# Performance work log

Hardware: AMD Instinct MI355X
Metric: run time of the kernel (lower is better)

The kernel has to match this reference:

```python
import jax, jax.numpy as jnp
import numpy as np

WINDOW_SIZE = 128

def setup_inputs() -> dict:
    key = jax.random.key(0)
    kq, kk, kv = jax.random.split(key, 3)
    B, S, D = 4, 4096, 128
    q = jax.random.normal(kq, (B, S, D), dtype=jnp.float32)
    k = jax.random.normal(kk, (B, S, D), dtype=jnp.float32)
    v = jax.random.normal(kv, (B, S, D), dtype=jnp.float32)
    return {"q": q, "k": k, "v": v}

def reference(q, k, v):
    B, S, D = q.shape
    q = q / jnp.sqrt(jnp.asarray(D, q.dtype))
    # band mask: tril(window_size-1) & triu(-(window_size-1)) == |i - j| <= window_size-1
    i = jax.lax.broadcasted_iota(jnp.int32, (S, S), 0)
    j = jax.lax.broadcasted_iota(jnp.int32, (S, S), 1)
    mask = jnp.abs(i - j) <= (WINDOW_SIZE - 1)
    scores = jnp.einsum('bqd,bkd->bqk', q, k)  # [B,S,S]
    scores = jnp.where(mask, scores, jnp.asarray(-1e9, scores.dtype))
    weights = jax.nn.softmax(scores, axis=-1)
    return jnp.einsum('bqk,bkd->bqd', weights, v)
```

## Files before the change

### kernel.cpp

```cpp
#include <hip/hip_runtime.h>


typedef __attribute__((ext_vector_type(8))) _Float16 half8;
typedef __attribute__((ext_vector_type(2))) __fp16 fp16x2;
typedef __attribute__((ext_vector_type(4))) float floatx4;

#define MFMA_F16(a, b, c) __builtin_amdgcn_mfma_f32_16x16x32_f16(a, b, c, 0, 0, 0)

constexpr int S_ = 4096, D_ = 128, W_ = 127;
constexpr int BQ = 64, BK = 64;
constexpr int PST = 72;
constexpr int OST = 132;

union SMem {
  struct {
    _Float16 Kh[2][BK * D_];
    _Float16 Vt[2][D_ * BK];
    _Float16 Ps[4][16 * PST];
  } a;
  struct {
    float Om[8][16 * OST];
    float l_[8][16];
  } b;
};

__device__ __forceinline__ unsigned pk2(float a, float b) {
  union { fp16x2 h; unsigned u; } c;
  c.h = __builtin_amdgcn_cvt_pkrtz(a, b);
  return c.u;
}

__device__ __forceinline__ void gll16(const _Float16* g, _Float16* l) {
  __builtin_amdgcn_global_load_lds(
      (const __attribute__((address_space(1))) void*)g,
      (__attribute__((address_space(3))) void*)l, 16, 0, 0);
}

__global__ __launch_bounds__(256, 4)
void prep_kernel(const float* __restrict__ kg, const float* __restrict__ vg,
                 _Float16* __restrict__ K16, _Float16* __restrict__ Vt16)
{
  __shared__ __align__(16) _Float16 Vs[BK * D_];
  const int t  = threadIdx.x;
  const int bb = blockIdx.x >> 6;
  const int c  = blockIdx.x & 63;
  const size_t base = ((size_t)bb * S_ + c * 64) * D_;

#pragma unroll
  for (int j = 0; j < 4; ++j) {
    const int id = t + 256 * j;
    const int s = id >> 4, blk = id & 15;
    const float* src = kg + base + s * D_ + blk * 8;
    float4 a  = *(const float4*)src;
    float4 b2 = *(const float4*)(src + 4);
    uint4 w;
    w.x = pk2(a.x, a.y);  w.y = pk2(a.z, a.w);
    w.z = pk2(b2.x, b2.y); w.w = pk2(b2.z, b2.w);
    *(uint4*)(K16 + base + s * D_ + 8 * (blk ^ (s & 7))) = w;
  }

  const int vr = t >> 5, vc = t & 31;
  float4 vf[8];
#pragma unroll
  for (int u = 0; u < 8; ++u)
    vf[u] = *(const float4*)(vg + base + (8 * vr + u) * D_ + 4 * vc);
#pragma unroll
  for (int i = 0; i < 4; ++i) {
    uint4 tv;
    tv.x = pk2(((const float*)&vf[0])[i], ((const float*)&vf[1])[i]);
    tv.y = pk2(((const float*)&vf[2])[i], ((const float*)&vf[3])[i]);
    tv.z = pk2(((const float*)&vf[4])[i], ((const float*)&vf[5])[i]);
    tv.w = pk2(((const float*)&vf[6])[i], ((const float*)&vf[7])[i]);
    const int d = 4 * vc + i;
    *(uint4*)(&Vs[d * 64 + 8 * (vr ^ (d & 7))]) = tv;
  }
  __syncthreads();
  _Float16* vdst = Vt16 + (size_t)(bb * 64 + c) * (D_ * 64);
#pragma unroll
  for (int i = 0; i < 4; ++i) {
    const int id2 = t + 256 * i;
    *(uint4*)(vdst + id2 * 8) = *(const uint4*)(&Vs[id2 * 8]);
  }
}

__global__ __launch_bounds__(512, 2)
void swa_v6_kernel(const float* __restrict__ qg,
                   const _Float16* __restrict__ K16,
                   const _Float16* __restrict__ Vt16,
                   float* __restrict__ og)
{
  __shared__ __align__(16) SMem sm;
  const int tid  = threadIdx.x;
  const int lane = tid & 63;
  const int wave = tid >> 6;
  const int lx   = lane & 15;
  const int quad = lane >> 4;
  const int tile = wave & 3;
  const int par  = wave >> 2;

  const int bid = blockIdx.x;
  const int lid = (bid & 7) * 32 + (bid >> 3);
  const int bb  = lid >> 6;
  const int q0  = (lid & 63) * BQ;

  const float* qb = qg + (size_t)bb * S_ * D_;
  float*       ob = og + (size_t)bb * S_ * D_;

  const int qrow = q0 + 16 * tile + lx;
  half8 qh[4], ql[4];
#pragma unroll
  for (int ks = 0; ks < 4; ++ks) {
    const float* p = qb + (size_t)qrow * D_ + 32 * ks + 8 * quad;
#pragma unroll
    for (int j = 0; j < 8; ++j) {
      float f = p[j];
      _Float16 h = (_Float16)f;
      qh[ks][j] = h;
      ql[ks][j] = (_Float16)(f - (float)h);
    }
  }

  floatx4 o[8];
#pragma unroll
  for (int dt = 0; dt < 8; ++dt) o[dt] = (floatx4){0.f, 0.f, 0.f, 0.f};
  float lp[4] = {0.f, 0.f, 0.f, 0.f};

  const int kstart = (q0 > W_) ? (q0 - W_) : 0;
  int kend = q0 + BQ - 1 + W_;
  if (kend > S_ - 1) kend = S_ - 1;
  const int c0 = kstart >> 6, c1 = kend >> 6;

  const int ilo = q0 + 16 * tile, ihi = ilo + 15;
  const float C1 = 0.12751727f, C2 = -5.7707802f;

  const int wk = (wave < 4) ? wave : (wave - 4);

  {
    const int b0 = c0 & 1;
    const _Float16* kcb = K16 + ((size_t)bb * S_ + c0 * 64) * D_;
    const _Float16* vcb = Vt16 + (size_t)(bb * 64 + c0) * (D_ * 64);
#pragma unroll
    for (int i = 0; i < 4; ++i) {
      const int ofs = (wk * 4 + i) * 512;
      if (wave < 4) gll16(kcb + ofs + lane * 8, &sm.a.Kh[b0][ofs]);
      else          gll16(vcb + ofs + lane * 8, &sm.a.Vt[b0][ofs]);
    }
  }

  for (int c = c0; c <= c1; ++c) {
    const int buf = c & 1;
    asm volatile("s_waitcnt vmcnt(0)" ::: "memory");
    __builtin_amdgcn_s_barrier();
    asm volatile("" ::: "memory");

    if (c < c1) {
      const _Float16* kcb = K16 + ((size_t)bb * S_ + (c + 1) * 64) * D_;
      const _Float16* vcb = Vt16 + (size_t)(bb * 64 + (c + 1)) * (D_ * 64);
#pragma unroll
      for (int i = 0; i < 4; ++i) {
        const int ofs = (wk * 4 + i) * 512;
        if (wave < 4) gll16(kcb + ofs + lane * 8, &sm.a.Kh[buf ^ 1][ofs]);
        else          gll16(vcb + ofs + lane * 8, &sm.a.Vt[buf ^ 1][ofs]);
      }
    }

    if (((c - c0) & 1) != par) continue;
    const int kc = c * BK;
    if (kc + BK - 1 < ilo - W_ || kc > ihi + W_) continue;

    floatx4 acc[4];
#pragma unroll
    for (int ct = 0; ct < 4; ++ct) acc[ct] = (floatx4){0.f, 0.f, 0.f, 0.f};
#pragma unroll
    for (int ks = 0; ks < 4; ++ks) {
#pragma unroll
      for (int ct = 0; ct < 4; ++ct) {
        const int row = 16 * ct + lx;
        half8 bfr = *(const half8*)(
            &sm.a.Kh[buf][row * D_ + 8 * ((4 * ks + quad) ^ (lx & 7))]);
        acc[ct] = MFMA_F16(qh[ks], bfr, acc[ct]);
        acc[ct] = MFMA_F16(ql[ks], bfr, acc[ct]);
      }
    }

    const int ibase = q0 + 16 * tile + 4 * quad;
#pragma unroll
    for (int r = 0; r < 4; ++r) {
      const int i = ibase + r;
      float psum = 0.f;
#pragma unroll
      for (int ct = 0; ct < 4; ++ct) {
        const int col = kc + 16 * ct + lx;
        const bool v = (unsigned)(col - i + W_) <= (unsigned)(2 * W_);
        const float e = __builtin_amdgcn_exp2f(__builtin_fmaf(acc[ct][r], C1, C2));
        const float p = v ? e : 0.f;
        psum += p;
        sm.a.Ps[tile][(4 * quad + r) * PST + 16 * ct + lx] = (_Float16)p;
      }
      lp[r] += psum;
    }
    asm volatile("s_waitcnt lgkmcnt(0)" ::: "memory");
    half8 pa0 = *(const half8*)(&sm.a.Ps[tile][lx * PST + 8 * quad]);
    half8 pa1 = *(const half8*)(&sm.a.Ps[tile][lx * PST + 32 + 8 * quad]);

#pragma unroll
    for (int dt = 0; dt < 8; ++dt) {
      const int d = 16 * dt + lx;
      half8 v0 = *(const half8*)(&sm.a.Vt[buf][d * 64 + 8 * (quad ^ (d & 7))]);
      half8 v1 = *(const half8*)(&sm.a.Vt[buf][d * 64 + 8 * ((4 + quad) ^ (d & 7))]);
      o[dt] = MFMA_F16(pa0, v0, o[dt]);
      o[dt] = MFMA_F16(pa1, v1, o[dt]);
    }
  }

#pragma unroll
  for (int r = 0; r < 4; ++r) {
    float s = lp[r];
    s += __shfl_xor(s, 1);
    s += __shfl_xor(s, 2);
    s += __shfl_xor(s, 4);
    s += __shfl_xor(s, 8);
    lp[r] = s;
  }

  __syncthreads();
#pragma unroll
  for (int dt = 0; dt < 8; ++dt)
#pragma unroll
    for (int r = 0; r < 4; ++r)
      sm.b.Om[wave][(4 * quad + r) * OST + 16 * dt + lx] = o[dt][r];
  if (lx == 0) {
#pragma unroll
    for (int r = 0; r < 4; ++r) sm.b.l_[wave][4 * quad + r] = lp[r];
  }
  __syncthreads();

  const int row = tid >> 3, cd = tid & 7;
  const int tl = row >> 4, r16 = row & 15;
  const float inv = 1.f / (sm.b.l_[tl][r16] + sm.b.l_[tl + 4][r16]);
  const float* Oa = &sm.b.Om[tl][r16 * OST + 16 * cd];
  const float* Ob = &sm.b.Om[tl + 4][r16 * OST + 16 * cd];
  float* dst = ob + (size_t)(q0 + row) * D_ + 16 * cd;
#pragma unroll
  for (int t = 0; t < 4; ++t) {
    float4 xa = *(const float4*)(Oa + 4 * t);
    float4 xb = *(const float4*)(Ob + 4 * t);
    float4 r4;
    r4.x = (xa.x + xb.x) * inv;
    r4.y = (xa.y + xb.y) * inv;
    r4.z = (xa.z + xb.z) * inv;
    r4.w = (xa.w + xb.w) * inv;
    *(float4*)(dst + 4 * t) = r4;
  }
}

extern "C" void kernel_launch(void* const* d_in, const int* in_sizes, int n_in,
                              void* d_out, int out_size, void* d_ws, size_t ws_size,
                              hipStream_t stream) {
  const float* q = (const float*)d_in[0];
  const float* k = (const float*)d_in[1];
  const float* v = (const float*)d_in[2];
  float* out = (float*)d_out;

  const int B = in_sizes[0] / (S_ * D_);
  _Float16* K16  = (_Float16*)d_ws;
  _Float16* Vt16 = (_Float16*)d_ws + (size_t)B * S_ * D_;

  prep_kernel<<<dim3(B * (S_ / BK)), dim3(256), 0, stream>>>(k, v, K16, Vt16);
  swa_v6_kernel<<<dim3(B * (S_ / BQ)), dim3(512), 0, stream>>>(q, K16, Vt16, out);
}
```

Baseline: 89.57 us.

## Fuse K/V fp16 conversion into attention kernel with register-staged prefetch

Removes the separate prep kernel that converted K and V to fp16 (with V transposed) in a global workspace. The attention kernel now loads fp32 K/V chunks into registers one chunk ahead, then converts, swizzles and writes them to LDS at the start of the next iteration. This drops one launch and a global round trip of the fp16 copies. In exchange each block redoes the conversion for its overlapping window (about three chunks per block), uses more registers, and puts more LDS-store work on the critical path. Q is now loaded with float4 vector loads.

```diff
diff --git a/kernel.cpp b/kernel.cpp
--- a/kernel.cpp
+++ b/kernel.cpp
@@ -30,63 +30,56 @@
   return c.u;
 }
 
-__device__ __forceinline__ void gll16(const _Float16* g, _Float16* l) {
-  __builtin_amdgcn_global_load_lds(
-      (const __attribute__((address_space(1))) void*)g,
-      (__attribute__((address_space(3))) void*)l, 16, 0, 0);
-}
-
-__global__ __launch_bounds__(256, 4)
-void prep_kernel(const float* __restrict__ kg, const float* __restrict__ vg,
-                 _Float16* __restrict__ K16, _Float16* __restrict__ Vt16)
-{
-  __shared__ __align__(16) _Float16 Vs[BK * D_];
-  const int t  = threadIdx.x;
-  const int bb = blockIdx.x >> 6;
-  const int c  = blockIdx.x & 63;
-  const size_t base = ((size_t)bb * S_ + c * 64) * D_;
-
-#pragma unroll
-  for (int j = 0; j < 4; ++j) {
-    const int id = t + 256 * j;
-    const int s = id >> 4, blk = id & 15;
-    const float* src = kg + base + s * D_ + blk * 8;
-    float4 a  = *(const float4*)src;
-    float4 b2 = *(const float4*)(src + 4);
-    uint4 w;
-    w.x = pk2(a.x, a.y);  w.y = pk2(a.z, a.w);
-    w.z = pk2(b2.x, b2.y); w.w = pk2(b2.z, b2.w);
-    *(uint4*)(K16 + base + s * D_ + 8 * (blk ^ (s & 7))) = w;
-  }
-
-  const int vr = t >> 5, vc = t & 31;
-  float4 vf[8];
-#pragma unroll
-  for (int u = 0; u < 8; ++u)
-    vf[u] = *(const float4*)(vg + base + (8 * vr + u) * D_ + 4 * vc);
-#pragma unroll
-  for (int i = 0; i < 4; ++i) {
-    uint4 tv;
-    tv.x = pk2(((const float*)&vf[0])[i], ((const float*)&vf[1])[i]);
-    tv.y = pk2(((const float*)&vf[2])[i], ((const float*)&vf[3])[i]);
-    tv.z = pk2(((const float*)&vf[4])[i], ((const float*)&vf[5])[i]);
-    tv.w = pk2(((const float*)&vf[6])[i], ((const float*)&vf[7])[i]);
-    const int d = 4 * vc + i;
-    *(uint4*)(&Vs[d * 64 + 8 * (vr ^ (d & 7))]) = tv;
-  }
-  __syncthreads();
-  _Float16* vdst = Vt16 + (size_t)(bb * 64 + c) * (D_ * 64);
-#pragma unroll
-  for (int i = 0; i < 4; ++i) {
-    const int id2 = t + 256 * i;
-    *(uint4*)(vdst + id2 * 8) = *(const uint4*)(&Vs[id2 * 8]);
-  }
-}
+#define ISSUE(cc) do {                                                        \
+    if (isK) {                                                                \
+      const float* kc_ = kb + (size_t)(cc) * (BK * D_);                       \
+      _Pragma("unroll")                                                       \
+      for (int j = 0; j < 4; ++j) {                                           \
+        const int id = tid + 256 * j;                                         \
+        const int s = id >> 4, blk = id & 15;                                 \
+        const float* src = kc_ + s * D_ + blk * 8;                            \
+        st[2 * j]     = *(const float4*)src;                                  \
+        st[2 * j + 1] = *(const float4*)(src + 4);                            \
+      }                                                                       \
+    } else {                                                                  \
+      const float* vc_ = vb + (size_t)(cc) * (BK * D_);                       \
+      _Pragma("unroll")                                                       \
+      for (int u = 0; u < 8; ++u)                                             \
+        st[u] = *(const float4*)(vc_ + (8 * vw + u) * D_ + 4 * vcg);          \
+    }                                                                         \
+  } while (0)
+
+#define COMMIT(bf) do {                                                       \
+    if (isK) {                                                                \
+      _Pragma("unroll")                                                       \
+      for (int j = 0; j < 4; ++j) {                                           \
+        const int id = tid + 256 * j;                                         \
+        const int s = id >> 4, blk = id & 15;                                 \
+        uint4 wv;                                                             \
+        wv.x = pk2(st[2 * j].x, st[2 * j].y);                                 \
+        wv.y = pk2(st[2 * j].z, st[2 * j].w);                                 \
+        wv.z = pk2(st[2 * j + 1].x, st[2 * j + 1].y);                         \
+        wv.w = pk2(st[2 * j + 1].z, st[2 * j + 1].w);                         \
+        *(uint4*)(&sm.a.Kh[bf][s * D_ + 8 * (blk ^ (s & 7))]) = wv;           \
+      }                                                                       \
+    } else {                                                                  \
+      _Pragma("unroll")                                                       \
+      for (int i = 0; i < 4; ++i) {                                           \
+        uint4 tv;                                                             \
+        tv.x = pk2(((const float*)&st[0])[i], ((const float*)&st[1])[i]);     \
+        tv.y = pk2(((const float*)&st[2])[i], ((const float*)&st[3])[i]);     \
+        tv.z = pk2(((const float*)&st[4])[i], ((const float*)&st[5])[i]);     \
+        tv.w = pk2(((const float*)&st[6])[i], ((const float*)&st[7])[i]);     \
+        const int d = 4 * vcg + i;                                            \
+        *(uint4*)(&sm.a.Vt[bf][d * 64 + 8 * (vw ^ (d & 7))]) = tv;            \
+      }                                                                       \
+    }                                                                         \
+  } while (0)
 
 __global__ __launch_bounds__(512, 2)
-void swa_v6_kernel(const float* __restrict__ qg,
-                   const _Float16* __restrict__ K16,
-                   const _Float16* __restrict__ Vt16,
+void swa_v7_kernel(const float* __restrict__ qg,
+                   const float* __restrict__ kg,
+                   const float* __restrict__ vg,
                    float* __restrict__ og)
 {
   __shared__ __align__(16) SMem sm;
@@ -104,19 +97,29 @@
   const int q0  = (lid & 63) * BQ;
 
   const float* qb = qg + (size_t)bb * S_ * D_;
+  const float* kb = kg + (size_t)bb * S_ * D_;
+  const float* vb = vg + (size_t)bb * S_ * D_;
   float*       ob = og + (size_t)bb * S_ * D_;
+
+  const bool isK = (wave < 4);
+  const int  t2  = tid & 255;
+  const int  vw  = t2 & 7;
+  const int  vcg = t2 >> 3;
+  float4 st[8];
 
   const int qrow = q0 + 16 * tile + lx;
   half8 qh[4], ql[4];
 #pragma unroll
   for (int ks = 0; ks < 4; ++ks) {
     const float* p = qb + (size_t)qrow * D_ + 32 * ks + 8 * quad;
+    float4 f0 = *(const float4*)p;
+    float4 f1 = *(const float4*)(p + 4);
+    float fa[8] = {f0.x, f0.y, f0.z, f0.w, f1.x, f1.y, f1.z, f1.w};
 #pragma unroll
     for (int j = 0; j < 8; ++j) {
-      float f = p[j];
-      _Float16 h = (_Float16)f;
+      _Float16 h = (_Float16)fa[j];
       qh[ks][j] = h;
-      ql[ks][j] = (_Float16)(f - (float)h);
+      ql[ks][j] = (_Float16)(fa[j] - (float)h);
     }
   }
 
@@ -133,36 +136,17 @@
   const int ilo = q0 + 16 * tile, ihi = ilo + 15;
   const float C1 = 0.12751727f, C2 = -5.7707802f;
 
-  const int wk = (wave < 4) ? wave : (wave - 4);
-
-  {
-    const int b0 = c0 & 1;
-    const _Float16* kcb = K16 + ((size_t)bb * S_ + c0 * 64) * D_;
-    const _Float16* vcb = Vt16 + (size_t)(bb * 64 + c0) * (D_ * 64);
-#pragma unroll
-    for (int i = 0; i < 4; ++i) {
-      const int ofs = (wk * 4 + i) * 512;
-      if (wave < 4) gll16(kcb + ofs + lane * 8, &sm.a.Kh[b0][ofs]);
-      else          gll16(vcb + ofs + lane * 8, &sm.a.Vt[b0][ofs]);
-    }
-  }
+  ISSUE(c0);
 
   for (int c = c0; c <= c1; ++c) {
     const int buf = c & 1;
-    asm volatile("s_waitcnt vmcnt(0)" ::: "memory");
+
+    COMMIT(buf);
+    asm volatile("s_waitcnt lgkmcnt(0)" ::: "memory");
     __builtin_amdgcn_s_barrier();
     asm volatile("" ::: "memory");
 
-    if (c < c1) {
-      const _Float16* kcb = K16 + ((size_t)bb * S_ + (c + 1) * 64) * D_;
-      const _Float16* vcb = Vt16 + (size_t)(bb * 64 + (c + 1)) * (D_ * 64);
-#pragma unroll
-      for (int i = 0; i < 4; ++i) {
-        const int ofs = (wk * 4 + i) * 512;
-        if (wave < 4) gll16(kcb + ofs + lane * 8, &sm.a.Kh[buf ^ 1][ofs]);
-        else          gll16(vcb + ofs + lane * 8, &sm.a.Vt[buf ^ 1][ofs]);
-      }
-    }
+    if (c < c1) ISSUE(c + 1);
 
     if (((c - c0) & 1) != par) continue;
     const int kc = c * BK;
@@ -257,15 +241,13 @@
 extern "C" void kernel_launch(void* const* d_in, const int* in_sizes, int n_in,
                               void* d_out, int out_size, void* d_ws, size_t ws_size,
                               hipStream_t stream) {
+  (void)d_ws; (void)ws_size;
   const float* q = (const float*)d_in[0];
   const float* k = (const float*)d_in[1];
   const float* v = (const float*)d_in[2];
   float* out = (float*)d_out;
 
   const int B = in_sizes[0] / (S_ * D_);
-  _Float16* K16  = (_Float16*)d_ws;
-  _Float16* Vt16 = (_Float16*)d_ws + (size_t)B * S_ * D_;
-
-  prep_kernel<<<dim3(B * (S_ / BK)), dim3(256), 0, stream>>>(k, v, K16, Vt16);
-  swa_v6_kernel<<<dim3(B * (S_ / BQ)), dim3(512), 0, stream>>>(q, K16, Vt16, out);
+
+  swa_v7_kernel<<<dim3(B * (S_ / BQ)), dim3(512), 0, stream>>>(q, k, v, out);
 }
```

New measurement: 92.00 us. 1.03x slower.

## Split each key chunk between wave groups by 32-key halves instead of alternating chunks

Applied to the files above, without the earlier changes.

Before, the two wave groups took alternating 64-key chunks, so when a block spans an odd number of chunks one group does more work than the other. Now both groups process every staged chunk, each computing QK^T, softmax weights and the PV product for its own 32-key half. The band-mask skip test also works at 32-key granularity, so halves that lie entirely outside a tile's window can be skipped. This trades halved MFMA work per chunk per wave for better balance between the groups and finer skipping, at the cost of less instruction-level work per barrier interval.

```diff
diff --git a/kernel.cpp b/kernel.cpp
--- a/kernel.cpp
+++ b/kernel.cpp
@@ -84,7 +84,7 @@
 }
 
 __global__ __launch_bounds__(512, 2)
-void swa_v6_kernel(const float* __restrict__ qg,
+void swa_v8_kernel(const float* __restrict__ qg,
                    const _Float16* __restrict__ K16,
                    const _Float16* __restrict__ Vt16,
                    float* __restrict__ og)
@@ -164,22 +164,23 @@
       }
     }
 
-    if (((c - c0) & 1) != par) continue;
     const int kc = c * BK;
-    if (kc + BK - 1 < ilo - W_ || kc > ihi + W_) continue;
-
-    floatx4 acc[4];
-#pragma unroll
-    for (int ct = 0; ct < 4; ++ct) acc[ct] = (floatx4){0.f, 0.f, 0.f, 0.f};
+    const int klo = kc + 32 * par;
+    if (klo + 31 < ilo - W_ || klo > ihi + W_) continue;
+
+    floatx4 acc[2];
+#pragma unroll
+    for (int h = 0; h < 2; ++h) acc[h] = (floatx4){0.f, 0.f, 0.f, 0.f};
 #pragma unroll
     for (int ks = 0; ks < 4; ++ks) {
 #pragma unroll
-      for (int ct = 0; ct < 4; ++ct) {
+      for (int h = 0; h < 2; ++h) {
+        const int ct = 2 * par + h;
         const int row = 16 * ct + lx;
         half8 bfr = *(const half8*)(
             &sm.a.Kh[buf][row * D_ + 8 * ((4 * ks + quad) ^ (lx & 7))]);
-        acc[ct] = MFMA_F16(qh[ks], bfr, acc[ct]);
-        acc[ct] = MFMA_F16(ql[ks], bfr, acc[ct]);
+        acc[h] = MFMA_F16(qh[ks], bfr, acc[h]);
+        acc[h] = MFMA_F16(ql[ks], bfr, acc[h]);
       }
     }
 
@@ -189,10 +190,11 @@
       const int i = ibase + r;
       float psum = 0.f;
 #pragma unroll
-      for (int ct = 0; ct < 4; ++ct) {
+      for (int h = 0; h < 2; ++h) {
+        const int ct = 2 * par + h;
         const int col = kc + 16 * ct + lx;
         const bool v = (unsigned)(col - i + W_) <= (unsigned)(2 * W_);
-        const float e = __builtin_amdgcn_exp2f(__builtin_fmaf(acc[ct][r], C1, C2));
+        const float e = __builtin_amdgcn_exp2f(__builtin_fmaf(acc[h][r], C1, C2));
         const float p = v ? e : 0.f;
         psum += p;
         sm.a.Ps[tile][(4 * quad + r) * PST + 16 * ct + lx] = (_Float16)p;
@@ -200,16 +202,14 @@
       lp[r] += psum;
     }
     asm volatile("s_waitcnt lgkmcnt(0)" ::: "memory");
-    half8 pa0 = *(const half8*)(&sm.a.Ps[tile][lx * PST + 8 * quad]);
-    half8 pa1 = *(const half8*)(&sm.a.Ps[tile][lx * PST + 32 + 8 * quad]);
+    half8 pa = *(const half8*)(&sm.a.Ps[tile][lx * PST + 32 * par + 8 * quad]);
 
 #pragma unroll
     for (int dt = 0; dt < 8; ++dt) {
       const int d = 16 * dt + lx;
-      half8 v0 = *(const half8*)(&sm.a.Vt[buf][d * 64 + 8 * (quad ^ (d & 7))]);
-      half8 v1 = *(const half8*)(&sm.a.Vt[buf][d * 64 + 8 * ((4 + quad) ^ (d & 7))]);
-      o[dt] = MFMA_F16(pa0, v0, o[dt]);
-      o[dt] = MFMA_F16(pa1, v1, o[dt]);
+      half8 vf = *(const half8*)(
+          &sm.a.Vt[buf][d * 64 + 8 * ((4 * par + quad) ^ (d & 7))]);
+      o[dt] = MFMA_F16(pa, vf, o[dt]);
     }
   }
 
@@ -267,5 +267,5 @@
   _Float16* Vt16 = (_Float16*)d_ws + (size_t)B * S_ * D_;
 
   prep_kernel<<<dim3(B * (S_ / BK)), dim3(256), 0, stream>>>(k, v, K16, Vt16);
-  swa_v6_kernel<<<dim3(B * (S_ / BQ)), dim3(512), 0, stream>>>(q, K16, Vt16, out);
-}
+  swa_v8_kernel<<<dim3(B * (S_ / BQ)), dim3(512), 0, stream>>>(q, K16, Vt16, out);
+}
```

New measurement: 87.84 us. Within noise of the previous version (-1.9%).
